# Kernel tuning notes

Measured on AMD Instinct MI355X. Metric: run time of the kernel, lower is better.

## Reference

```python
import jax, jax.numpy as jnp
import numpy as np

D = 1024       # d_model
H = 16         # n_heads
N = 8          # ortho_dim
NSKEW = N * (N - 1) // 2
MAX_ANGLE = 0.5
B, T = 4, 4096
IDX_I, IDX_J = np.triu_indices(N, k=1)


def setup_inputs() -> dict:
    key = jax.random.key(0)
    ks = jax.random.split(key, 8)
    s = 0.02
    w = lambda k, shape: jax.random.normal(k, shape, jnp.float32) * s
    return {
        "x": jax.random.normal(ks[0], (B, T, D), jnp.float32),
        "W_skew": w(ks[1], (D, H * NSKEW)),
        "W_k": w(ks[2], (D, H * N)),
        "W_v": w(ks[3], (D, H * N)),
        "W_q": w(ks[4], (D, H * N)),
        "W_beta": w(ks[5], (D, H)),
        "b_beta": w(ks[6], (H,)),
        "W_o": w(ks[7], (H * N, D)),
    }


def _forward(x, W_skew, W_k, W_v, W_q, W_beta, b_beta, W_o):
    Bb, Tt, _ = x.shape
    # skew-symmetric generator -> rotation O_t = expm(skew)
    skew_flat = MAX_ANGLE * jnp.tanh(x @ W_skew).reshape(Bb, Tt, H, NSKEW)
    skew = jnp.zeros((Bb, Tt, H, N, N), x.dtype)
    skew = skew.at[..., IDX_I, IDX_J].set(skew_flat)
    skew = skew.at[..., IDX_J, IDX_I].set(-skew_flat)
    O = jax.vmap(jax.scipy.linalg.expm)(skew.reshape(-1, N, N)).reshape(Bb, Tt, H, N, N)

    k = (x @ W_k).reshape(Bb, Tt, H, N)
    k = k / jnp.maximum(jnp.linalg.norm(k, axis=-1, keepdims=True), 1e-6)
    v = (x @ W_v).reshape(Bb, Tt, H, N)
    q = (x @ W_q).reshape(Bb, Tt, H, N)
    beta = jax.nn.sigmoid(x @ W_beta + b_beta)  # [B,T,H]

    def step(c, inp):
        O_t, k_t, v_t, b_t, q_t = inp  # [B,H,n,n], [B,H,n], ...
        # rotation conjugation: O c O^T
        c_rot = jnp.einsum('bhij,bhjk,bhlk->bhil', O_t, c, O_t)
        # rank-1 erase: c_rot - beta * k (k^T c_rot); rank-1 write: + beta * k v^T
        kc = jnp.einsum('bhi,bhij->bhj', k_t, c_rot)
        b = b_t[..., None, None]
        c_new = c_rot - b * k_t[..., None] * kc[..., None, :] + b * k_t[..., None] * v_t[..., None, :]
        o_t = jnp.einsum('bhi,bhij->bhj', q_t, c_new)  # readout q . c_t
        return c_new, o_t

    c0 = jnp.zeros((Bb, H, N, N), x.dtype)
    tfirst = lambda a: jnp.moveaxis(a, 1, 0)
    _, o = jax.lax.scan(step, c0, (tfirst(O), tfirst(k), tfirst(v), tfirst(beta), tfirst(q)))
    o = jnp.moveaxis(o, 0, 1).reshape(Bb, Tt, H * N)
    return o @ W_o


def reference(x, W_skew, W_k, W_v, W_q, W_beta, b_beta, W_o):
    return _forward(x, W_skew, W_k, W_v, W_q, W_beta, b_beta, W_o)
```

## Files before the change

### kernel.cpp

```cpp
#include <hip/hip_runtime.h>

typedef unsigned short u16;
typedef unsigned int u32;
typedef __attribute__((ext_vector_type(4))) float f32x4;
typedef __attribute__((ext_vector_type(8))) short short8;
typedef __attribute__((ext_vector_type(4))) unsigned int u32x4;

#define DEV __device__ __forceinline__

DEV float bf2f(u16 u){ union{u32 i; float f;} x; x.i = ((u32)u)<<16; return x.f; }
DEV u16 f2bf(float f){ union{u32 i; float f;} x; x.f = f; u32 r = x.i + 0x7fffu + ((x.i>>16)&1u); return (u16)(r>>16); }

union U8 { u16 u[8]; short8 s; };

DEV void gl16(const u16* g, u16* l){
  __builtin_amdgcn_global_load_lds(
      (const __attribute__((address_space(1))) u32*)g,
      (__attribute__((address_space(3))) u32*)l, 16, 0, 0);
}

DEV float fast_htanh(float v){
  float vc = fminf(fmaxf(v, -15.f), 15.f);
  float e = __expf(2.f*vc);
  return 0.5f*(e - 1.f)*__builtin_amdgcn_rcpf(e + 1.f);
}
DEV float fast_sigmoid(float v){
  float e = __expf(-v);
  return __builtin_amdgcn_rcpf(1.f + e);
}

__global__ __launch_bounds__(256) void splitx_kernel(const float* __restrict__ x,
    u16* __restrict__ xh, u16* __restrict__ xl)
{
  size_t base = ((size_t)blockIdx.x*256 + threadIdx.x) * 8;
  f32x4 a = *(const f32x4*)(x + base), b = *(const f32x4*)(x + base + 4);
  U8 h, l;
  #pragma unroll
  for (int e=0;e<4;e++){
    u16 hh = f2bf(a[e]); h.u[e]   = hh; l.u[e]   = f2bf(a[e] - bf2f(hh));
    u16 gg = f2bf(b[e]); h.u[4+e] = gg; l.u[4+e] = f2bf(b[e] - bf2f(gg));
  }
  *(short8*)(xh + base) = h.s;
  *(short8*)(xl + base) = l.s;
}

__global__ __launch_bounds__(256) void concat_kernel(
    const float* __restrict__ Wskew, const float* __restrict__ Wk, const float* __restrict__ Wv,
    const float* __restrict__ Wq, const float* __restrict__ Wbeta, const float* __restrict__ Wo,
    u16* __restrict__ Wh, u16* __restrict__ Wl, u16* __restrict__ WoT)
{
  int idx = blockIdx.x*256 + threadIdx.x;
  if (idx < 896*1024){
    int n = idx >> 10, kk = idx & 1023;
    float v;
    if (n < 448)      v = Wskew[kk*448 + n];
    else if (n < 576) v = Wk[kk*128 + (n-448)];
    else if (n < 704) v = Wv[kk*128 + (n-576)];
    else if (n < 832) v = Wq[kk*128 + (n-704)];
    else if (n < 848) v = Wbeta[kk*16 + (n-832)];
    else              v = 0.f;
    u16 h = f2bf(v);
    Wh[idx] = h;
    Wl[idx] = f2bf(v - bf2f(h));
  } else {
    int r = idx - 896*1024;
    int n = r >> 7, kk = r & 127;
    WoT[r] = f2bf(Wo[kk*1024 + n]);
  }
}

__global__ __launch_bounds__(256) void gemm_proj_kernel(
    const u16* __restrict__ Ah, const u16* __restrict__ Al,
    const u16* __restrict__ Bh, const u16* __restrict__ Bl,
    float* __restrict__ C, const float* __restrict__ bias)
{
  __shared__ u16 L[2*4*4096];
  const int tid = threadIdx.x;
  const int wave = tid >> 6;
  const int lane = tid & 63;
  const int quad = lane >> 4, l15 = lane & 15;
  const int m0 = blockIdx.x * 128, n0 = blockIdx.y * 128;
  const bool full = (blockIdx.y < 4);
  const int wm = (wave >> 1) * 64, wn = (wave & 1) * 64;
  const bool wantLow = full && !(blockIdx.y == 3 && wn == 64);
  const bool skipBl1 = (blockIdx.y == 3);
  const int K = 1024, ldc = 896;
  const int sr = tid >> 2;
  const int sc = tid & 3;
  const int fS = (sr & 3) ^ ((sr >> 2) & 3);
  const int scS = ((sc ^ fS) << 3);
  const size_t gA0 = (size_t)(m0 + sr)*K + scS, gA1 = gA0 + (size_t)64*K;
  const size_t gB0 = (size_t)(n0 + sr)*K + scS, gB1 = gB0 + (size_t)64*K;
  const int d0 = tid*8, d1 = d0 + 2048;
  const int fR = (l15 & 3) ^ ((l15 >> 2) & 3);
  const int rq = ((quad ^ fR) << 3);

  auto STAGE = [&](int buf, int kb){
    u16* Lb = L + buf*16384;
    gl16(Ah + gA0 + kb, Lb + d0);
    gl16(Ah + gA1 + kb, Lb + d1);
    gl16(Bh + gB0 + kb, Lb + 4096 + d0);
    gl16(Bh + gB1 + kb, Lb + 4096 + d1);
    if (full){
      gl16(Al + gA0 + kb, Lb + 8192 + d0);
      gl16(Al + gA1 + kb, Lb + 8192 + d1);
      gl16(Bl + gB0 + kb, Lb + 12288 + d0);
      if (!skipBl1) gl16(Bl + gB1 + kb, Lb + 12288 + d1);
    }
  };

  f32x4 acc[4][4] = {};
  STAGE(0, 0);
  __syncthreads();
  int cur = 0;
  for (int kb = 0; kb < K; kb += 32){
    if (kb + 32 < K) STAGE(cur^1, kb + 32);
    u16* Lb = L + cur*16384;
    short8 afh[4], bfh[4];
    #pragma unroll
    for (int mi=0;mi<4;mi++) afh[mi] = *(const short8*)&Lb[(wm + mi*16 + l15)*32 + rq];
    #pragma unroll
    for (int ni=0;ni<4;ni++) bfh[ni] = *(const short8*)&Lb[4096 + (wn + ni*16 + l15)*32 + rq];
    #pragma unroll
    for (int mi=0;mi<4;mi++)
      #pragma unroll
      for (int ni=0;ni<4;ni++)
        acc[mi][ni] = __builtin_amdgcn_mfma_f32_16x16x32_bf16(afh[mi], bfh[ni], acc[mi][ni], 0,0,0);
    if (wantLow){
      short8 afl[4], bfl[4];
      #pragma unroll
      for (int mi=0;mi<4;mi++) afl[mi] = *(const short8*)&Lb[8192 + (wm + mi*16 + l15)*32 + rq];
      #pragma unroll
      for (int ni=0;ni<4;ni++) bfl[ni] = *(const short8*)&Lb[12288 + (wn + ni*16 + l15)*32 + rq];
      #pragma unroll
      for (int mi=0;mi<4;mi++)
        #pragma unroll
        for (int ni=0;ni<4;ni++){
          acc[mi][ni] = __builtin_amdgcn_mfma_f32_16x16x32_bf16(afh[mi], bfl[ni], acc[mi][ni], 0,0,0);
          acc[mi][ni] = __builtin_amdgcn_mfma_f32_16x16x32_bf16(afl[mi], bfh[ni], acc[mi][ni], 0,0,0);
        }
    }
    __syncthreads();
    cur ^= 1;
  }
  #pragma unroll
  for (int mi=0;mi<4;mi++){
    #pragma unroll
    for (int ni=0;ni<4;ni++){
      const int col = n0 + wn + ni*16 + l15;
      const int rb_ = m0 + wm + mi*16 + quad*4;
      #pragma unroll
      for (int r=0;r<4;r++){
        float v = acc[mi][ni][r];
        const int row = rb_ + r;
        if (col < 448) v = fast_htanh(v);
        else if (col >= 832 && col < 848) v = fast_sigmoid(v + bias[col-832]);
        C[(size_t)row*ldc + col] = v;
      }
    }
  }
}

__global__ __launch_bounds__(256) void gemm_out_kernel(
    const u16* __restrict__ A, const u16* __restrict__ Bt, float* __restrict__ C)
{
  __shared__ u16 L[2*2*4096];
  const int tid = threadIdx.x;
  const int wave = tid >> 6;
  const int lane = tid & 63;
  const int quad = lane >> 4, l15 = lane & 15;
  const int m0 = blockIdx.x * 128, n0 = blockIdx.y * 128;
  const int wm = (wave >> 1) * 64, wn = (wave & 1) * 64;
  const int K = 128, ldc = 1024;
  const int sr = tid >> 2;
  const int sc = tid & 3;
  const int fS = (sr & 3) ^ ((sr >> 2) & 3);
  const int scS = ((sc ^ fS) << 3);
  const size_t gA0 = (size_t)(m0 + sr)*K + scS, gA1 = gA0 + (size_t)64*K;
  const size_t gB0 = (size_t)(n0 + sr)*K + scS, gB1 = gB0 + (size_t)64*K;
  const int d0 = tid*8, d1 = d0 + 2048;
  const int fR = (l15 & 3) ^ ((l15 >> 2) & 3);
  const int rq = ((quad ^ fR) << 3);

  auto STAGE = [&](int buf, int kb){
    u16* Lb = L + buf*8192;
    gl16(A  + gA0 + kb, Lb + d0);
    gl16(A  + gA1 + kb, Lb + d1);
    gl16(Bt + gB0 + kb, Lb + 4096 + d0);
    gl16(Bt + gB1 + kb, Lb + 4096 + d1);
  };

  f32x4 acc[4][4] = {};
  STAGE(0, 0);
  __syncthreads();
  int cur = 0;
  for (int kb = 0; kb < K; kb += 32){
    if (kb + 32 < K) STAGE(cur^1, kb + 32);
    u16* Lb = L + cur*8192;
    short8 af[4], bf8[4];
    #pragma unroll
    for (int mi=0;mi<4;mi++) af[mi] = *(const short8*)&Lb[(wm + mi*16 + l15)*32 + rq];
    #pragma unroll
    for (int ni=0;ni<4;ni++) bf8[ni] = *(const short8*)&Lb[4096 + (wn + ni*16 + l15)*32 + rq];
    #pragma unroll
    for (int mi=0;mi<4;mi++)
      #pragma unroll
      for (int ni=0;ni<4;ni++)
        acc[mi][ni] = __builtin_amdgcn_mfma_f32_16x16x32_bf16(af[mi], bf8[ni], acc[mi][ni], 0,0,0);
    __syncthreads();
    cur ^= 1;
  }
  #pragma unroll
  for (int mi=0;mi<4;mi++)
    #pragma unroll
    for (int ni=0;ni<4;ni++){
      const int col = n0 + wn + ni*16 + l15;
      const int rb_ = m0 + wm + mi*16 + quad*4;
      #pragma unroll
      for (int r=0;r<4;r++)
        C[(size_t)(rb_ + r)*ldc + col] = acc[mi][ni][r];
    }
}

__device__ constexpr int TRI_I[28] = {0,0,0,0,0,0,0, 1,1,1,1,1,1, 2,2,2,2,2, 3,3,3,3, 4,4,4, 5,5, 6};
__device__ constexpr int TRI_J[28] = {1,2,3,4,5,6,7, 2,3,4,5,6,7, 3,4,5,6,7, 4,5,6,7, 5,6,7, 6,7, 7};

__global__ __launch_bounds__(64, 1) void expm_scan_kernel(float* __restrict__ proj, float* __restrict__ OR)
{
  __shared__ float S0[16*64*4];
  const int t = threadIdx.x;
  const int s = blockIdx.x >> 6, c = blockIdx.x & 63;
  const int b = s >> 4, h = s & 15;
  const int row = b*4096 + c*64 + t;
  float* pr = proj + (size_t)row*896;
  const float* sk = pr + h*28;

  float v[28];
  {
    f32x4 vv[7];
    #pragma unroll
    for (int i=0;i<7;i++) vv[i] = *(const f32x4*)(sk + 4*i);
    #pragma unroll
    for (int i=0;i<28;i++) v[i] = vv[i>>2][i&3] * 0.0625f;
  }

  float M[64], T[64];
  auto bmul = [&](const float* Min, float* Tout){
    #pragma unroll
    for (int i=0;i<8;i++){
      #pragma unroll
      for (int cc=0;cc<8;cc++){
        float acc = 0.f;
        #pragma unroll
        for (int a=0;a<8;a++){
          if (a == i) continue;
          const int k = (i<a) ? (i*7 - (i*(i-1))/2 + a - i - 1)
                              : (a*7 - (a*(a-1))/2 + i - a - 1);
          if (i<a) acc = fmaf( v[k], Min[a*8+cc], acc);
          else     acc = fmaf(-v[k], Min[a*8+cc], acc);
        }
        Tout[i*8+cc] = acc;
      }
    }
  };
  #pragma unroll
  for (int i=0;i<8;i++){
    #pragma unroll
    for (int jj=0;jj<8;jj++){
      float bv = 0.f;
      if (i < jj){ const int k = i*7 - (i*(i-1))/2 + jj - i - 1; bv =  v[k]; }
      if (i > jj){ const int k = jj*7 - (jj*(jj-1))/2 + i - jj - 1; bv = -v[k]; }
      M[i*8+jj] = bv*(1.f/6.f) + ((i==jj)?1.f:0.f);
    }
  }
  const float coef[5] = {0.2f, 0.25f, 1.f/3.f, 0.5f, 1.f};
  #pragma unroll
  for (int st=0; st<5; st++){
    bmul(M, T);
    #pragma unroll
    for (int i=0;i<8;i++)
      #pragma unroll
      for (int jj=0;jj<8;jj++)
        M[i*8+jj] = T[i*8+jj]*coef[st] + ((i==jj)?1.f:0.f);
  }
  #pragma unroll
  for (int sq=0; sq<4; sq++){
    #pragma unroll
    for (int i=0;i<8;i++)
      #pragma unroll
      for (int cc=0;cc<8;cc++){
        float acc = 0.f;
        #pragma unroll
        for (int a=0;a<8;a++) acc = fmaf(M[i*8+a], M[a*8+cc], acc);
        T[i*8+cc] = acc;
      }
    #pragma unroll
    for (int f=0;f<64;f++) M[f] = T[f];
  }
  #pragma unroll
  for (int j=0;j<16;j++){
    f32x4 w = {M[4*j], M[4*j+1], M[4*j+2], M[4*j+3]};
    *(f32x4*)&S0[(j*64 + t)*4] = w;
  }
  __syncthreads();

  #pragma unroll
  for (int d=0; d<6; d++){
    const int off = 1 << d;
    if (t >= off){
      float Q[64];
      #pragma unroll
      for (int j=0;j<16;j++){
        f32x4 x = *(const f32x4*)&S0[(j*64 + (t-off))*4];
        Q[4*j]=x[0]; Q[4*j+1]=x[1]; Q[4*j+2]=x[2]; Q[4*j+3]=x[3];
      }
      #pragma unroll
      for (int i=0;i<8;i++){
        float r[8];
        #pragma unroll
        for (int cc=0;cc<8;cc++){
          float acc = 0.f;
          #pragma unroll
          for (int a=0;a<8;a++) acc = fmaf(M[i*8+a], Q[a*8+cc], acc);
          r[cc] = acc;
        }
        #pragma unroll
        for (int cc=0;cc<8;cc++) M[i*8+cc] = r[cc];
      }
    }
    if (d < 5){
      #pragma unroll
      for (int j=0;j<16;j++){
        f32x4 w = {M[4*j], M[4*j+1], M[4*j+2], M[4*j+3]};
        *(f32x4*)&S0[(j*64 + t)*4] = w;
      }
      __syncthreads();
    }
  }

  float* dst = OR + ((size_t)s*4096 + (size_t)c*64 + t)*64;
  #pragma unroll
  for (int j=0;j<16;j++){
    const int rb = 4*(j&1), col = j>>1;
    f32x4 w = {M[(rb+0)*8 + col], M[(rb+1)*8 + col], M[(rb+2)*8 + col], M[(rb+3)*8 + col]};
    *(f32x4*)(dst + 4*j) = w;
  }

  float kk[8], vv2[8], qq[8];
  { f32x4 a = *(const f32x4*)(pr+448+h*8), b2 = *(const f32x4*)(pr+452+h*8);
    #pragma unroll
    for (int i=0;i<4;i++){ kk[i]=a[i]; kk[4+i]=b2[i]; } }
  { f32x4 a = *(const f32x4*)(pr+576+h*8), b2 = *(const f32x4*)(pr+580+h*8);
    #pragma unroll
    for (int i=0;i<4;i++){ vv2[i]=a[i]; vv2[4+i]=b2[i]; } }
  { f32x4 a = *(const f32x4*)(pr+704+h*8), b2 = *(const f32x4*)(pr+708+h*8);
    #pragma unroll
    for (int i=0;i<4;i++){ qq[i]=a[i]; qq[4+i]=b2[i]; } }
  float nn = 0.f;
  #pragma unroll
  for (int i=0;i<8;i++) nn = fmaf(kk[i],kk[i],nn);
  float inv = 1.f / fmaxf(sqrtf(nn), 1e-6f);
  #pragma unroll
  for (int i=0;i<8;i++) kk[i] *= inv;
  float uk[8], uv[8], uq[8];
  #pragma unroll
  for (int a=0;a<8;a++){
    float sk_=0.f, sv_=0.f, sq_=0.f;
    #pragma unroll
    for (int i=0;i<8;i++){
      float m = M[i*8+a];
      sk_ = fmaf(m, kk[i], sk_); sv_ = fmaf(m, vv2[i], sv_); sq_ = fmaf(m, qq[i], sq_);
    }
    uk[a]=sk_; uv[a]=sv_; uq[a]=sq_;
  }
  float beta = pr[832+h];
  float qk = 0.f;
  #pragma unroll
  for (int a=0;a<8;a++) qk = fmaf(uk[a], uq[a], qk);
  float* sip = pr + h*28;
  f32x4 w0={uk[0],uk[1],uk[2],uk[3]}, w1={uk[4],uk[5],uk[6],uk[7]};
  f32x4 w2={uv[0],uv[1],uv[2],uv[3]}, w3={uv[4],uv[5],uv[6],uv[7]};
  f32x4 w4={uq[0],uq[1],uq[2],uq[3]}, w5={uq[4],uq[5],uq[6],uq[7]};
  f32x4 w6={beta, qk, 0.f, 0.f};
  *(f32x4*)(sip)=w0; *(f32x4*)(sip+4)=w1; *(f32x4*)(sip+8)=w2; *(f32x4*)(sip+12)=w3;
  *(f32x4*)(sip+16)=w4; *(f32x4*)(sip+20)=w5; *(f32x4*)(sip+24)=w6;
}

DEV void load16(const float* p, f32x4* M){
  #pragma unroll
  for (int q=0;q<16;q++) M[q] = *(const f32x4*)(p + 4*q);
}
DEV void rm_matvec8(const f32x4* M16, const float* x, float* res){
  #pragma unroll
  for (int i=0;i<8;i++){
    float acc = 0.f;
    #pragma unroll
    for (int a=0;a<8;a++) acc = fmaf(M16[2*i + (a>>2)][a&3], x[a], acc);
    res[i] = acc;
  }
}
DEV void cm_matvec8(const f32x4* M16, const float* x, float* res){
  #pragma unroll
  for (int i=0;i<8;i++){
    float acc = 0.f;
    #pragma unroll
    for (int a=0;a<8;a++) acc = fmaf(M16[2*a + (i>>2)][i&3], x[a], acc);
    res[i] = acc;
  }
}

__global__ __launch_bounds__(64, 1) void chunkscan_kernel(const float* __restrict__ OR, float* __restrict__ Rbase)
{
  __shared__ float S[64*68];
  const int t = threadIdx.x;
  const int s = blockIdx.x;
  float M[64];
  const float* qs = OR + ((size_t)s*4096 + (size_t)t*64 + 63)*64;
  #pragma unroll
  for (int j=0;j<16;j++){
    f32x4 x = *(const f32x4*)(qs + 4*j);
    M[4*j]=x[0]; M[4*j+1]=x[1]; M[4*j+2]=x[2]; M[4*j+3]=x[3];
  }
  #pragma unroll
  for (int j=0;j<16;j++){
    f32x4 w = {M[4*j],M[4*j+1],M[4*j+2],M[4*j+3]};
    *(f32x4*)&S[t*68 + 4*j] = w;
  }
  __syncthreads();
  #pragma unroll
  for (int d=0; d<6; d++){
    const int off = 1 << d;
    if (t >= off){
      float Q[64];
      const float* p = &S[(t-off)*68];
      #pragma unroll
      for (int j=0;j<16;j++){
        f32x4 x = *(const f32x4*)(p + 4*j);
        Q[4*j]=x[0]; Q[4*j+1]=x[1]; Q[4*j+2]=x[2]; Q[4*j+3]=x[3];
      }
      float R[64];
      #pragma unroll
      for (int cc=0;cc<8;cc++)
        #pragma unroll
        for (int i=0;i<8;i++){
          float acc = 0.f;
          #pragma unroll
          for (int a=0;a<8;a++) acc = fmaf(M[a*8+i], Q[cc*8+a], acc);
          R[cc*8+i] = acc;
        }
      #pragma unroll
      for (int f=0;f<64;f++) M[f] = R[f];
    }
    if (d < 5){
      #pragma unroll
      for (int j=0;j<16;j++){
        f32x4 w = {M[4*j],M[4*j+1],M[4*j+2],M[4*j+3]};
        *(f32x4*)&S[t*68 + 4*j] = w;
      }
      __syncthreads();
    }
  }
  if (t < 63){
    float* dst = Rbase + ((size_t)s*64 + t + 1)*64;
    #pragma unroll
    for (int j=0;j<16;j++){
      f32x4 w = {M[4*j],M[4*j+1],M[4*j+2],M[4*j+3]};
      *(f32x4*)(dst + 4*j) = w;
    }
  }
  if (t == 0){
    float* dst = Rbase + (size_t)s*64*64;
    #pragma unroll
    for (int cc=0;cc<8;cc++)
      #pragma unroll
      for (int i=0;i<8;i++) dst[cc*8+i] = (i==cc) ? 1.f : 0.f;
  }
}

__global__ __launch_bounds__(256) void rotate_kvq_kernel(const float* __restrict__ Rbase,
    float* __restrict__ proj)
{
  int tid = blockIdx.x*256 + threadIdx.x;
  int s = tid >> 12, t = tid & 4095;
  int c = t >> 6;
  int b = s >> 4, h = s & 15;
  int row = b*4096 + t;
  float* sip = proj + (size_t)row*896 + h*28;
  float uk[8], uv[8], uq[8];
  { f32x4 a = *(const f32x4*)(sip),    b2 = *(const f32x4*)(sip+4);
    #pragma unroll
    for (int i=0;i<4;i++){ uk[i]=a[i]; uk[4+i]=b2[i]; } }
  { f32x4 a = *(const f32x4*)(sip+8),  b2 = *(const f32x4*)(sip+12);
    #pragma unroll
    for (int i=0;i<4;i++){ uv[i]=a[i]; uv[4+i]=b2[i]; } }
  { f32x4 a = *(const f32x4*)(sip+16), b2 = *(const f32x4*)(sip+20);
    #pragma unroll
    for (int i=0;i<4;i++){ uq[i]=a[i]; uq[4+i]=b2[i]; } }
  f32x4 M[16];
  load16(Rbase + ((size_t)s*64 + c)*64, M);
  float kt[8], vt[8], qt[8];
  rm_matvec8(M, uk, kt);
  rm_matvec8(M, uv, vt);
  rm_matvec8(M, uq, qt);
  f32x4 w0={kt[0],kt[1],kt[2],kt[3]}, w1={kt[4],kt[5],kt[6],kt[7]};
  f32x4 w2={vt[0],vt[1],vt[2],vt[3]}, w3={vt[4],vt[5],vt[6],vt[7]};
  f32x4 w4={qt[0],qt[1],qt[2],qt[3]}, w5={qt[4],qt[5],qt[6],qt[7]};
  *(f32x4*)(sip)=w0; *(f32x4*)(sip+4)=w1; *(f32x4*)(sip+8)=w2; *(f32x4*)(sip+12)=w3;
  *(f32x4*)(sip+16)=w4; *(f32x4*)(sip+20)=w5;
}

__global__ __launch_bounds__(256) void scan_pass1_kernel(const float* __restrict__ proj,
    float* __restrict__ Mbuf, float* __restrict__ wbuf)
{
  int tid = blockIdx.x*256 + threadIdx.x;
  int task = tid >> 3, j = tid & 7;
  int s = task >> 8, c = task & 255;
  int b = s >> 4, h = s & 15;
  const float* rec = proj + ((size_t)b*4096 + (size_t)c*16)*896 + h*28;
  float m[8], w[8];
  #pragma unroll
  for (int i=0;i<8;i++){ m[i] = (i==j)?1.f:0.f; w[i] = 0.f; }
  f32x4 k0 = *(const f32x4*)(rec), k1 = *(const f32x4*)(rec+4);
  float vt = rec[8+j];
  float beta = rec[24];
  for (int tt=0; tt<16; tt++){
    const float* pn = rec + (size_t)(tt+1)*896;
    f32x4 nk0 = *(const f32x4*)(pn), nk1 = *(const f32x4*)(pn+4);
    float nvt = pn[8+j];
    float nbeta = pn[24];
    float s1, s2;
    s1 = ((k0[0]*m[0] + k0[1]*m[1]) + (k0[2]*m[2] + k0[3]*m[3]))
       + ((k1[0]*m[4] + k1[1]*m[5]) + (k1[2]*m[6] + k1[3]*m[7]));
    s2 = ((k0[0]*w[0] + k0[1]*w[1]) + (k0[2]*w[2] + k0[3]*w[3]))
       + ((k1[0]*w[4] + k1[1]*w[5]) + (k1[2]*w[6] + k1[3]*w[7]));
    float c1 = -beta*s1, c2 = beta*(vt - s2);
    #pragma unroll
    for (int i=0;i<4;i++){ m[i] = fmaf(k0[i], c1, m[i]); m[4+i] = fmaf(k1[i], c1, m[4+i]); }
    #pragma unroll
    for (int i=0;i<4;i++){ w[i] = fmaf(k0[i], c2, w[i]); w[4+i] = fmaf(k1[i], c2, w[4+i]); }
    k0=nk0; k1=nk1; vt=nvt; beta=nbeta;
  }
  float* md = Mbuf + (size_t)task*64 + j*8;
  float* wd = wbuf + (size_t)task*64 + j*8;
  f32x4 m0={m[0],m[1],m[2],m[3]}, m1={m[4],m[5],m[6],m[7]};
  f32x4 w0={w[0],w[1],w[2],w[3]}, w1={w[4],w[5],w[6],w[7]};
  *(f32x4*)(md) = m0; *(f32x4*)(md+4) = m1;
  *(f32x4*)(wd) = w0; *(f32x4*)(wd+4) = w1;
}

__global__ __launch_bounds__(512) void scan_mid_kernel(const float* __restrict__ Mbuf,
    const float* __restrict__ wbuf, float* __restrict__ dstart)
{
  __shared__ float SM[256*68];
  __shared__ float SW[256*68];
  const int tid = threadIdx.x;
  const int c = tid >> 1, g = tid & 1;
  const int s = blockIdx.x;
  const size_t base = (size_t)s*256*64;
  const float* mp = Mbuf + base + (size_t)c*64 + 32*g;
  const float* wp = wbuf + base + (size_t)c*64 + 32*g;
  float W[32];
  {
    float* sm = &SM[c*68 + 32*g];
    float* sw = &SW[c*68 + 32*g];
    #pragma unroll
    for (int j=0;j<8;j++){
      f32x4 a = *(const f32x4*)(mp + 4*j);
      f32x4 b = *(const f32x4*)(wp + 4*j);
      *(f32x4*)(sm + 4*j) = a;
      *(f32x4*)(sw + 4*j) = b;
      W[4*j]=b[0]; W[4*j+1]=b[1]; W[4*j+2]=b[2]; W[4*j+3]=b[3];
    }
  }
  __syncthreads();
  for (int d=0; d<8; d++){
    const int off = 1 << d;
    const bool act = (c >= off);
    float Mo[64], pM[32], pW[32];
    if (act){
      const float* om = &SM[c*68];
      #pragma unroll
      for (int j=0;j<16;j++){
        f32x4 x = *(const f32x4*)(om + 4*j);
        Mo[4*j]=x[0]; Mo[4*j+1]=x[1]; Mo[4*j+2]=x[2]; Mo[4*j+3]=x[3];
      }
      const float* qm = &SM[(c-off)*68 + 32*g];
      const float* qw = &SW[(c-off)*68 + 32*g];
      #pragma unroll
      for (int j=0;j<8;j++){
        f32x4 x = *(const f32x4*)(qm + 4*j);
        f32x4 y = *(const f32x4*)(qw + 4*j);
        pM[4*j]=x[0]; pM[4*j+1]=x[1]; pM[4*j+2]=x[2]; pM[4*j+3]=x[3];
        pW[4*j]=y[0]; pW[4*j+1]=y[1]; pW[4*j+2]=y[2]; pW[4*j+3]=y[3];
      }
    }
    __syncthreads();
    if (act){
      float nM[32], nW[32];
      #pragma unroll
      for (int cl=0; cl<4; cl++){
        #pragma unroll
        for (int i=0;i<8;i++){
          float aM = 0.f, aW = 0.f;
          #pragma unroll
          for (int a=0;a<8;a++){
            aM = fmaf(Mo[a*8+i], pM[cl*8+a], aM);
            aW = fmaf(Mo[a*8+i], pW[cl*8+a], aW);
          }
          nM[cl*8+i] = aM;
          nW[cl*8+i] = aW + W[cl*8+i];
        }
      }
      float* sm = &SM[c*68 + 32*g];
      float* sw = &SW[c*68 + 32*g];
      #pragma unroll
      for (int j=0;j<8;j++){
        f32x4 x = {nM[4*j], nM[4*j+1], nM[4*j+2], nM[4*j+3]};
        f32x4 y = {nW[4*j], nW[4*j+1], nW[4*j+2], nW[4*j+3]};
        *(f32x4*)(sm + 4*j) = x;
        *(f32x4*)(sw + 4*j) = y;
      }
      #pragma unroll
      for (int f=0;f<32;f++) W[f] = nW[f];
    }
    __syncthreads();
  }
  if (c < 255){
    float* dd = dstart + base + (size_t)(c+1)*64 + 32*g;
    #pragma unroll
    for (int j=0;j<8;j++){
      f32x4 y = {W[4*j],W[4*j+1],W[4*j+2],W[4*j+3]};
      *(f32x4*)(dd + 4*j) = y;
    }
  }
  if (c == 0){
    float* dd = dstart + base + 32*g;
    f32x4 z = {0.f,0.f,0.f,0.f};
    #pragma unroll
    for (int j=0;j<8;j++) *(f32x4*)(dd + 4*j) = z;
  }
}

__global__ __launch_bounds__(256) void scan_pass2_kernel(const float* __restrict__ proj,
    const float* __restrict__ dstart, float* __restrict__ oo)
{
  int tid = blockIdx.x*256 + threadIdx.x;
  int task = tid >> 3, j = tid & 7;
  int s = task >> 8, c = task & 255;
  int b = s >> 4, h = s & 15;
  const float* rec = proj + ((size_t)b*4096 + (size_t)c*16)*896 + h*28;
  float* op = oo + (((size_t)s*4096 + (size_t)c*16)*8) + j;
  float d[8];
  { const float* ds = dstart + (size_t)task*64 + j*8;
    f32x4 a = *(const f32x4*)(ds), b2 = *(const f32x4*)(ds+4);
    #pragma unroll
    for (int i=0;i<4;i++){ d[i]=a[i]; d[4+i]=b2[i]; } }
  f32x4 k0 = *(const f32x4*)(rec),    k1 = *(const f32x4*)(rec+4);
  f32x4 q0 = *(const f32x4*)(rec+16), q1 = *(const f32x4*)(rec+20);
  f32x4 mb = *(const f32x4*)(rec+24);
  float vt = rec[8+j];
  for (int tt=0; tt<16; tt++){
    const float* pn = rec + (size_t)(tt+1)*896;
    f32x4 nk0 = *(const f32x4*)(pn),    nk1 = *(const f32x4*)(pn+4);
    f32x4 nq0 = *(const f32x4*)(pn+16), nq1 = *(const f32x4*)(pn+20);
    f32x4 nmb = *(const f32x4*)(pn+24);
    float nvt = pn[8+j];
    float kd, qd;
    kd = ((k0[0]*d[0] + k0[1]*d[1]) + (k0[2]*d[2] + k0[3]*d[3]))
       + ((k1[0]*d[4] + k1[1]*d[5]) + (k1[2]*d[6] + k1[3]*d[7]));
    qd = ((q0[0]*d[0] + q0[1]*d[1]) + (q0[2]*d[2] + q0[3]*d[3]))
       + ((q1[0]*d[4] + q1[1]*d[5]) + (q1[2]*d[6] + q1[3]*d[7]));
    float w_ = mb[0] * (vt - kd);
    #pragma unroll
    for (int i=0;i<4;i++){ d[i] = fmaf(k0[i], w_, d[i]); d[4+i] = fmaf(k1[i], w_, d[4+i]); }
    op[(size_t)tt*8] = fmaf(mb[1], w_, qd);
    k0=nk0; k1=nk1; q0=nq0; q1=nq1; mb=nmb; vt=nvt;
  }
}

__global__ __launch_bounds__(256) void rotout_kernel(const float* __restrict__ OR, const float* __restrict__ Rbase,
                                                     const float* __restrict__ oo, u16* __restrict__ obf)
{
  int tid = blockIdx.x*256 + threadIdx.x;
  int s = tid >> 12, t = tid & 4095;
  int c = t >> 6;
  int b = s >> 4, h = s & 15;
  int row = b*4096 + t;
  float u[8];
  { const float* up = oo + ((size_t)s*4096 + t)*8;
    f32x4 a = *(const f32x4*)(up), b2 = *(const f32x4*)(up+4);
    #pragma unroll
    for (int i=0;i<4;i++){ u[i]=a[i]; u[4+i]=b2[i]; } }
  f32x4 M[16];
  load16(Rbase + ((size_t)s*64 + c)*64, M);
  float w[8];
  cm_matvec8(M, u, w);
  load16(OR + ((size_t)s*4096 + t)*64, M);
  float o[8];
  cm_matvec8(M, w, o);
  u32 p0 = (u32)f2bf(o[0]) | ((u32)f2bf(o[1])<<16);
  u32 p1 = (u32)f2bf(o[2]) | ((u32)f2bf(o[3])<<16);
  u32 p2 = (u32)f2bf(o[4]) | ((u32)f2bf(o[5])<<16);
  u32 p3 = (u32)f2bf(o[6]) | ((u32)f2bf(o[7])<<16);
  u32x4 pk = {p0,p1,p2,p3};
  *(u32x4*)(void*)(obf + (size_t)row*128 + h*8) = pk;
}

extern "C" void kernel_launch(void* const* d_in, const int* in_sizes, int n_in,
                              void* d_out, int out_size, void* d_ws, size_t ws_size,
                              hipStream_t stream)
{
  const float* x     = (const float*)d_in[0];
  const float* Wskew = (const float*)d_in[1];
  const float* Wk    = (const float*)d_in[2];
  const float* Wv    = (const float*)d_in[3];
  const float* Wq    = (const float*)d_in[4];
  const float* Wbeta = (const float*)d_in[5];
  const float* bbeta = (const float*)d_in[6];
  const float* Wo    = (const float*)d_in[7];

  char* w = (char*)d_ws; size_t off = 0;
  auto alloc = [&](size_t bytes)->void*{ void* p = w + off; off += (bytes + 255) & ~(size_t)255; return p; };
  u16*   Wh     = (u16*)  alloc((size_t)896*1024*2);
  u16*   Wl     = (u16*)  alloc((size_t)896*1024*2);
  u16*   WoT    = (u16*)  alloc((size_t)1024*128*2);
  float* proj   = (float*)alloc((size_t)16384*896*4);
  float* OR     = (float*)alloc((size_t)262144*64*4);
  float* Rbase  = (float*)alloc((size_t)64*64*64*4);
  float* oo     = (float*)alloc((size_t)262144*8*4);
  float* Mbuf   = (float*)alloc((size_t)16384*64*4);
  float* wbuf   = (float*)alloc((size_t)16384*64*4);
  float* dstart = (float*)alloc((size_t)16384*64*4);
  u16*   xh     = (u16*)OR;
  u16*   xl     = xh + (size_t)16384*1024;
  u16*   obf    = (u16*)proj;

  hipLaunchKernelGGL(splitx_kernel, dim3(8192), dim3(256), 0, stream, x, xh, xl);
  hipLaunchKernelGGL(concat_kernel, dim3(4096), dim3(256), 0, stream,
                     Wskew, Wk, Wv, Wq, Wbeta, Wo, Wh, Wl, WoT);
  hipLaunchKernelGGL(gemm_proj_kernel, dim3(128,7), dim3(256), 0, stream,
                     xh, xl, Wh, Wl, proj, bbeta);
  hipLaunchKernelGGL(expm_scan_kernel, dim3(4096), dim3(64), 0, stream, proj, OR);
  hipLaunchKernelGGL(chunkscan_kernel, dim3(64), dim3(64), 0, stream, OR, Rbase);
  hipLaunchKernelGGL(rotate_kvq_kernel, dim3(1024), dim3(256), 0, stream, Rbase, proj);
  hipLaunchKernelGGL(scan_pass1_kernel, dim3(512), dim3(256), 0, stream, proj, Mbuf, wbuf);
  hipLaunchKernelGGL(scan_mid_kernel, dim3(64), dim3(512), 0, stream, Mbuf, wbuf, dstart);
  hipLaunchKernelGGL(scan_pass2_kernel, dim3(512), dim3(256), 0, stream, proj, dstart, oo);
  hipLaunchKernelGGL(rotout_kernel, dim3(1024), dim3(256), 0, stream, OR, Rbase, oo, obf);
  hipLaunchKernelGGL(gemm_out_kernel, dim3(128,8), dim3(256), 0, stream,
                     obf, WoT, (float*)d_out);
}
```

Baseline: 374.2 us.

## Split expm and prefix-product matmuls across thread pairs in expm_scan

Each 8x8 rotation matrix is now computed by two lanes, each owning four rows, with the partner's rows exchanged through xor-shuffles during the Taylor and squaring matmuls. The block grows to 128 threads, and the intra-chunk prefix product reads the neighbour matrix from padded row-major shared memory. The aim is to roughly halve per-thread register pressure and FMA chain length so occupancy and latency hiding improve. The cost is extra shuffles, an additional barrier per scan step, and split global writes.

```diff
diff --git a/kernel.cpp b/kernel.cpp
--- a/kernel.cpp
+++ b/kernel.cpp
@@ -225,165 +225,187 @@
 __device__ constexpr int TRI_I[28] = {0,0,0,0,0,0,0, 1,1,1,1,1,1, 2,2,2,2,2, 3,3,3,3, 4,4,4, 5,5, 6};
 __device__ constexpr int TRI_J[28] = {1,2,3,4,5,6,7, 2,3,4,5,6,7, 3,4,5,6,7, 4,5,6,7, 5,6,7, 6,7, 7};
 
-__global__ __launch_bounds__(64, 1) void expm_scan_kernel(float* __restrict__ proj, float* __restrict__ OR)
-{
-  __shared__ float S0[16*64*4];
-  const int t = threadIdx.x;
+DEV void pair_matmul(const float XA[4][4], const float XB[4][4], const float Mm[4][8], float Tm[4][8]){
+  float Yo[4][8];
+  #pragma unroll
+  for (int r=0;r<4;r++)
+    #pragma unroll
+    for (int jj=0;jj<8;jj++) Yo[r][jj] = __shfl_xor(Mm[r][jj], 1);
+  #pragma unroll
+  for (int i=0;i<4;i++)
+    #pragma unroll
+    for (int jj=0;jj<8;jj++){
+      float acc = 0.f;
+      #pragma unroll
+      for (int r=0;r<4;r++){ acc = fmaf(XA[i][r], Mm[r][jj], acc); acc = fmaf(XB[i][r], Yo[r][jj], acc); }
+      Tm[i][jj] = acc;
+    }
+}
+
+__global__ __launch_bounds__(128, 2) void expm_scan_kernel(float* __restrict__ proj, float* __restrict__ OR)
+{
+  __shared__ float S[64*68];
+  const int tid = threadIdx.x;
+  const int m = tid >> 1;
+  const int p = tid & 1;
   const int s = blockIdx.x >> 6, c = blockIdx.x & 63;
   const int b = s >> 4, h = s & 15;
-  const int row = b*4096 + c*64 + t;
+  const int row = b*4096 + c*64 + m;
   float* pr = proj + (size_t)row*896;
   const float* sk = pr + h*28;
 
-  float v[28];
-  {
-    f32x4 vv[7];
-    #pragma unroll
-    for (int i=0;i<7;i++) vv[i] = *(const f32x4*)(sk + 4*i);
-    #pragma unroll
-    for (int i=0;i<28;i++) v[i] = vv[i>>2][i&3] * 0.0625f;
-  }
-
-  float M[64], T[64];
-  auto bmul = [&](const float* Min, float* Tout){
-    #pragma unroll
-    for (int i=0;i<8;i++){
-      #pragma unroll
-      for (int cc=0;cc<8;cc++){
-        float acc = 0.f;
-        #pragma unroll
-        for (int a=0;a<8;a++){
-          if (a == i) continue;
-          const int k = (i<a) ? (i*7 - (i*(i-1))/2 + a - i - 1)
-                              : (a*7 - (a*(a-1))/2 + i - a - 1);
-          if (i<a) acc = fmaf( v[k], Min[a*8+cc], acc);
-          else     acc = fmaf(-v[k], Min[a*8+cc], acc);
-        }
-        Tout[i*8+cc] = acc;
-      }
-    }
-  };
-  #pragma unroll
-  for (int i=0;i<8;i++){
-    #pragma unroll
-    for (int jj=0;jj<8;jj++){
-      float bv = 0.f;
-      if (i < jj){ const int k = i*7 - (i*(i-1))/2 + jj - i - 1; bv =  v[k]; }
-      if (i > jj){ const int k = jj*7 - (jj*(jj-1))/2 + i - jj - 1; bv = -v[k]; }
-      M[i*8+jj] = bv*(1.f/6.f) + ((i==jj)?1.f:0.f);
-    }
-  }
+  float Bm[4][8];
+  #pragma unroll
+  for (int i=0;i<4;i++)
+    #pragma unroll
+    for (int jj=0;jj<8;jj++) Bm[i][jj] = 0.f;
+  #pragma unroll
+  for (int cc=0;cc<28;cc++){
+    const int ti = TRI_I[cc], tj = TRI_J[cc];
+    float v = sk[cc] * 0.0625f;
+    if (p==0){
+      if (ti < 4) Bm[ti][tj] = v;
+      if (tj < 4) Bm[tj][ti] = -v;
+    } else {
+      if (ti >= 4) Bm[ti-4][tj] = v;
+      if (tj >= 4) Bm[tj-4][ti] = -v;
+    }
+  }
+  float BA[4][4], BB[4][4];
+  #pragma unroll
+  for (int i=0;i<4;i++)
+    #pragma unroll
+    for (int r=0;r<4;r++){ float lo=Bm[i][r], hi=Bm[i][4+r]; BA[i][r] = p? hi: lo; BB[i][r] = p? lo: hi; }
+
+  float Mm[4][8], Tm[4][8];
+  #pragma unroll
+  for (int i=0;i<4;i++)
+    #pragma unroll
+    for (int jj=0;jj<8;jj++) Mm[i][jj] = Bm[i][jj]*(1.f/6.f) + (((4*p+i)==jj)?1.f:0.f);
   const float coef[5] = {0.2f, 0.25f, 1.f/3.f, 0.5f, 1.f};
   #pragma unroll
   for (int st=0; st<5; st++){
-    bmul(M, T);
-    #pragma unroll
-    for (int i=0;i<8;i++)
-      #pragma unroll
-      for (int jj=0;jj<8;jj++)
-        M[i*8+jj] = T[i*8+jj]*coef[st] + ((i==jj)?1.f:0.f);
+    pair_matmul(BA, BB, Mm, Tm);
+    #pragma unroll
+    for (int i=0;i<4;i++)
+      #pragma unroll
+      for (int jj=0;jj<8;jj++) Mm[i][jj] = Tm[i][jj]*coef[st] + (((4*p+i)==jj)?1.f:0.f);
   }
   #pragma unroll
   for (int sq=0; sq<4; sq++){
-    #pragma unroll
-    for (int i=0;i<8;i++)
-      #pragma unroll
-      for (int cc=0;cc<8;cc++){
-        float acc = 0.f;
-        #pragma unroll
-        for (int a=0;a<8;a++) acc = fmaf(M[i*8+a], M[a*8+cc], acc);
-        T[i*8+cc] = acc;
-      }
-    #pragma unroll
-    for (int f=0;f<64;f++) M[f] = T[f];
-  }
-  #pragma unroll
-  for (int j=0;j<16;j++){
-    f32x4 w = {M[4*j], M[4*j+1], M[4*j+2], M[4*j+3]};
-    *(f32x4*)&S0[(j*64 + t)*4] = w;
+    float MA[4][4], MB[4][4];
+    #pragma unroll
+    for (int i=0;i<4;i++)
+      #pragma unroll
+      for (int r=0;r<4;r++){ float lo=Mm[i][r], hi=Mm[i][4+r]; MA[i][r] = p? hi: lo; MB[i][r] = p? lo: hi; }
+    pair_matmul(MA, MB, Mm, Tm);
+    #pragma unroll
+    for (int i=0;i<4;i++)
+      #pragma unroll
+      for (int jj=0;jj<8;jj++) Mm[i][jj] = Tm[i][jj];
+  }
+
+  #pragma unroll
+  for (int i=0;i<4;i++){
+    f32x4 lo = {Mm[i][0],Mm[i][1],Mm[i][2],Mm[i][3]};
+    f32x4 hi = {Mm[i][4],Mm[i][5],Mm[i][6],Mm[i][7]};
+    *(f32x4*)&S[m*68 + (4*p+i)*8]     = lo;
+    *(f32x4*)&S[m*68 + (4*p+i)*8 + 4] = hi;
   }
   __syncthreads();
 
   #pragma unroll
   for (int d=0; d<6; d++){
     const int off = 1 << d;
-    if (t >= off){
-      float Q[64];
-      #pragma unroll
-      for (int j=0;j<16;j++){
-        f32x4 x = *(const f32x4*)&S0[(j*64 + (t-off))*4];
-        Q[4*j]=x[0]; Q[4*j+1]=x[1]; Q[4*j+2]=x[2]; Q[4*j+3]=x[3];
-      }
-      #pragma unroll
-      for (int i=0;i<8;i++){
-        float r[8];
+    float R[4][8];
+    if (m >= off){
+      const float* Q = &S[(m-off)*68];
+      #pragma unroll
+      for (int i=0;i<4;i++)
         #pragma unroll
-        for (int cc=0;cc<8;cc++){
-          float acc = 0.f;
-          #pragma unroll
-          for (int a=0;a<8;a++) acc = fmaf(M[i*8+a], Q[a*8+cc], acc);
-          r[cc] = acc;
+        for (int e=0;e<8;e++) R[i][e] = 0.f;
+      #pragma unroll
+      for (int a=0;a<8;a++){
+        f32x4 q0 = *(const f32x4*)(Q + a*8);
+        f32x4 q1 = *(const f32x4*)(Q + a*8 + 4);
+        #pragma unroll
+        for (int i=0;i<4;i++){
+          float mv = Mm[i][a];
+          R[i][0] = fmaf(mv, q0[0], R[i][0]); R[i][1] = fmaf(mv, q0[1], R[i][1]);
+          R[i][2] = fmaf(mv, q0[2], R[i][2]); R[i][3] = fmaf(mv, q0[3], R[i][3]);
+          R[i][4] = fmaf(mv, q1[0], R[i][4]); R[i][5] = fmaf(mv, q1[1], R[i][5]);
+          R[i][6] = fmaf(mv, q1[2], R[i][6]); R[i][7] = fmaf(mv, q1[3], R[i][7]);
         }
+      }
+    } else {
+      #pragma unroll
+      for (int i=0;i<4;i++)
         #pragma unroll
-        for (int cc=0;cc<8;cc++) M[i*8+cc] = r[cc];
-      }
+        for (int e=0;e<8;e++) R[i][e] = Mm[i][e];
     }
     if (d < 5){
-      #pragma unroll
-      for (int j=0;j<16;j++){
-        f32x4 w = {M[4*j], M[4*j+1], M[4*j+2], M[4*j+3]};
-        *(f32x4*)&S0[(j*64 + t)*4] = w;
-      }
       __syncthreads();
-    }
-  }
-
-  float* dst = OR + ((size_t)s*4096 + (size_t)c*64 + t)*64;
-  #pragma unroll
-  for (int j=0;j<16;j++){
-    const int rb = 4*(j&1), col = j>>1;
-    f32x4 w = {M[(rb+0)*8 + col], M[(rb+1)*8 + col], M[(rb+2)*8 + col], M[(rb+3)*8 + col]};
-    *(f32x4*)(dst + 4*j) = w;
-  }
-
-  float kk[8], vv2[8], qq[8];
-  { f32x4 a = *(const f32x4*)(pr+448+h*8), b2 = *(const f32x4*)(pr+452+h*8);
-    #pragma unroll
-    for (int i=0;i<4;i++){ kk[i]=a[i]; kk[4+i]=b2[i]; } }
-  { f32x4 a = *(const f32x4*)(pr+576+h*8), b2 = *(const f32x4*)(pr+580+h*8);
-    #pragma unroll
-    for (int i=0;i<4;i++){ vv2[i]=a[i]; vv2[4+i]=b2[i]; } }
-  { f32x4 a = *(const f32x4*)(pr+704+h*8), b2 = *(const f32x4*)(pr+708+h*8);
-    #pragma unroll
-    for (int i=0;i<4;i++){ qq[i]=a[i]; qq[4+i]=b2[i]; } }
-  float nn = 0.f;
-  #pragma unroll
-  for (int i=0;i<8;i++) nn = fmaf(kk[i],kk[i],nn);
+      if (m >= off){
+        #pragma unroll
+        for (int i=0;i<4;i++){
+          f32x4 lo = {R[i][0],R[i][1],R[i][2],R[i][3]};
+          f32x4 hi = {R[i][4],R[i][5],R[i][6],R[i][7]};
+          *(f32x4*)&S[m*68 + (4*p+i)*8]     = lo;
+          *(f32x4*)&S[m*68 + (4*p+i)*8 + 4] = hi;
+        }
+      }
+      __syncthreads();
+    }
+    #pragma unroll
+    for (int i=0;i<4;i++)
+      #pragma unroll
+      for (int e=0;e<8;e++) Mm[i][e] = R[i][e];
+  }
+
+  float* dst = OR + ((size_t)s*4096 + (size_t)c*64 + m)*64 + 4*p;
+  #pragma unroll
+  for (int a=0;a<8;a++){
+    f32x4 w = {Mm[0][a], Mm[1][a], Mm[2][a], Mm[3][a]};
+    *(f32x4*)(dst + a*8) = w;
+  }
+
+  f32x4 kv = *(const f32x4*)(pr + 448 + h*8 + 4*p);
+  f32x4 vv = *(const f32x4*)(pr + 576 + h*8 + 4*p);
+  f32x4 qv = *(const f32x4*)(pr + 704 + h*8 + 4*p);
+  float pnn = kv[0]*kv[0] + kv[1]*kv[1] + kv[2]*kv[2] + kv[3]*kv[3];
+  float nn = pnn + __shfl_xor(pnn, 1);
   float inv = 1.f / fmaxf(sqrtf(nn), 1e-6f);
-  #pragma unroll
-  for (int i=0;i<8;i++) kk[i] *= inv;
+  float kkv[4];
+  #pragma unroll
+  for (int i=0;i<4;i++) kkv[i] = kv[i]*inv;
   float uk[8], uv[8], uq[8];
   #pragma unroll
   for (int a=0;a<8;a++){
-    float sk_=0.f, sv_=0.f, sq_=0.f;
-    #pragma unroll
-    for (int i=0;i<8;i++){
-      float m = M[i*8+a];
-      sk_ = fmaf(m, kk[i], sk_); sv_ = fmaf(m, vv2[i], sv_); sq_ = fmaf(m, qq[i], sq_);
-    }
-    uk[a]=sk_; uv[a]=sv_; uq[a]=sq_;
-  }
-  float beta = pr[832+h];
+    float pk=0.f, pv=0.f, pq=0.f;
+    #pragma unroll
+    for (int i=0;i<4;i++){
+      float mv = Mm[i][a];
+      pk = fmaf(mv, kkv[i], pk); pv = fmaf(mv, vv[i], pv); pq = fmaf(mv, qv[i], pq);
+    }
+    uk[a] = pk + __shfl_xor(pk, 1);
+    uv[a] = pv + __shfl_xor(pv, 1);
+    uq[a] = pq + __shfl_xor(pq, 1);
+  }
+  float beta = pr[832 + h];
   float qk = 0.f;
   #pragma unroll
   for (int a=0;a<8;a++) qk = fmaf(uk[a], uq[a], qk);
   float* sip = pr + h*28;
-  f32x4 w0={uk[0],uk[1],uk[2],uk[3]}, w1={uk[4],uk[5],uk[6],uk[7]};
-  f32x4 w2={uv[0],uv[1],uv[2],uv[3]}, w3={uv[4],uv[5],uv[6],uv[7]};
-  f32x4 w4={uq[0],uq[1],uq[2],uq[3]}, w5={uq[4],uq[5],uq[6],uq[7]};
-  f32x4 w6={beta, qk, 0.f, 0.f};
-  *(f32x4*)(sip)=w0; *(f32x4*)(sip+4)=w1; *(f32x4*)(sip+8)=w2; *(f32x4*)(sip+12)=w3;
-  *(f32x4*)(sip+16)=w4; *(f32x4*)(sip+20)=w5; *(f32x4*)(sip+24)=w6;
+  if (p == 0){
+    f32x4 w0={uk[0],uk[1],uk[2],uk[3]}, w1={uk[4],uk[5],uk[6],uk[7]};
+    f32x4 w2={uv[0],uv[1],uv[2],uv[3]}, w3={uv[4],uv[5],uv[6],uv[7]};
+    *(f32x4*)(sip)    = w0; *(f32x4*)(sip+4)  = w1;
+    *(f32x4*)(sip+8)  = w2; *(f32x4*)(sip+12) = w3;
+  } else {
+    f32x4 w4={uq[0],uq[1],uq[2],uq[3]}, w5={uq[4],uq[5],uq[6],uq[7]};
+    f32x4 w6={beta, qk, 0.f, 0.f};
+    *(f32x4*)(sip+16) = w4; *(f32x4*)(sip+20) = w5; *(f32x4*)(sip+24) = w6;
+  }
 }
 
 DEV void load16(const float* p, f32x4* M){
@@ -740,7 +762,7 @@
                      Wskew, Wk, Wv, Wq, Wbeta, Wo, Wh, Wl, WoT);
   hipLaunchKernelGGL(gemm_proj_kernel, dim3(128,7), dim3(256), 0, stream,
                      xh, xl, Wh, Wl, proj, bbeta);
-  hipLaunchKernelGGL(expm_scan_kernel, dim3(4096), dim3(64), 0, stream, proj, OR);
+  hipLaunchKernelGGL(expm_scan_kernel, dim3(4096), dim3(128), 0, stream, proj, OR);
   hipLaunchKernelGGL(chunkscan_kernel, dim3(64), dim3(64), 0, stream, OR, Rbase);
   hipLaunchKernelGGL(rotate_kvq_kernel, dim3(1024), dim3(256), 0, stream, Rbase, proj);
   hipLaunchKernelGGL(scan_pass1_kernel, dim3(512), dim3(256), 0, stream, proj, Mbuf, wbuf);
```

Result: slower. 386.8 us (+3.4%).
